# Kernel optimization log

Hardware: AMD Instinct MI355X
Metric: run time of the kernel (lower is better)

## Reference

```python
import jax, jax.numpy as jnp
import numpy as np

B, E, H, F, L, A = 256, 1024, 1024, 2048, 196, 512
C_RATIO, H_RATIO = 0.5, 0.5


def setup_inputs() -> dict:
    key = jax.random.key(0)
    ks = jax.random.split(key, 20)
    u = lambda k, shape: jax.random.uniform(k, shape, jnp.float32, -0.1, 0.1)
    return {
        "xt": jax.random.normal(ks[0], (B, E), jnp.float32),
        "att_seq": jax.random.normal(ks[1], (B, L, F), jnp.float32),
        "h": jax.random.normal(ks[2], (B, H), jnp.float32),
        "c": jax.random.normal(ks[3], (B, H), jnp.float32),
        "Wi": u(ks[4], (4 * H, E)), "bi": u(ks[5], (4 * H,)),
        "Wh": u(ks[6], (4 * H, H)), "bh": u(ks[7], (4 * H,)),
        "Wz": u(ks[8], (4 * H, F)), "bz": u(ks[9], (4 * H,)),
        "Wa": u(ks[10], (A, F)), "ba": u(ks[11], (A,)),
        "Wha": u(ks[12], (A, H)), "bha": u(ks[13], (A,)),
        "Wo": u(ks[14], (1, A)), "bo": u(ks[15], (1,)),
    }


def reference(xt, att_seq, h, c, Wi, bi, Wh, bh, Wz, bz, Wa, ba, Wha, bha, Wo, bo):
    # attention scoring: tanh(att_2_att_h(att) + h_2_att_h(h)) -> scalar per location
    att_linear = jnp.einsum("blf,af->bla", att_seq, Wa) + ba          # [B,L,A]
    h_linear = h @ Wha.T + bha                                        # [B,A]
    att_h = jnp.tanh(att_linear + h_linear[:, None, :])               # [B,L,A]
    scores = jnp.einsum("bla,a->bl", att_h, Wo[0]) + bo[0]            # [B,L]
    w = jax.nn.softmax(scores, axis=-1)                               # [B,L]
    z = jnp.einsum("bl,blf->bf", w, att_seq)                          # [B,F] context

    # fused LSTM gates
    sums = (xt @ Wi.T + bi) + (h @ Wh.T + bh) + (z @ Wz.T + bz)       # [B,4H]
    i_g = jax.nn.sigmoid(sums[:, 0 * H:1 * H])
    f_g = jax.nn.sigmoid(sums[:, 1 * H:2 * H])
    o_g = jax.nn.sigmoid(sums[:, 2 * H:3 * H])
    g = jnp.tanh(sums[:, 3 * H:4 * H])

    # zoneout blending (training mode; dropout prob is 0 -> identity)
    next_c = c * C_RATIO + (1.0 - C_RATIO) * (f_g * c + i_g * g)
    next_h = h * H_RATIO + (1.0 - H_RATIO) * (o_g * jnp.tanh(next_c))
    return next_h, next_h, next_c  # (output, state_h, state_c)
```

## Files before the change

### kernel.cpp

```cpp
#include <hip/hip_runtime.h>

#define B_ 256
#define E_ 1024
#define H_ 1024
#define F_ 2048
#define L_ 196
#define A_ 512
#define ML (B_ * L_)

typedef __attribute__((ext_vector_type(8))) short short8;
typedef __attribute__((ext_vector_type(4))) float f32x4;

__device__ __forceinline__ unsigned short f2bf(float x) {
  unsigned u = __float_as_uint(x);
  unsigned r = (u + 0x7FFFu + ((u >> 16) & 1u)) >> 16;
  return (unsigned short)r;
}
__device__ __forceinline__ float fast_tanh(float x) {
  x = fminf(fmaxf(x, -15.f), 15.f);
  float e = __expf(2.f * x);
  return (e - 1.f) / (e + 1.f);
}
__device__ __forceinline__ float sigmoidf_(float x) {
  return 1.f / (1.f + __expf(-x));
}

#define GLOAD_LDS(gptr, lptr) \
  __builtin_amdgcn_global_load_lds( \
      (const __attribute__((address_space(1))) void*)(gptr), \
      (__attribute__((address_space(3))) void*)(lptr), 16, 0, 0)

#define SBAR() asm volatile("s_barrier" ::: "memory")

__global__ void cast_wx_k(const float* __restrict__ Wa, const float* __restrict__ Wha,
                          const float* __restrict__ Wi, const float* __restrict__ Wh,
                          const float* __restrict__ Wz, const float* __restrict__ xt,
                          const float* __restrict__ h,
                          unsigned short* __restrict__ WaB, unsigned short* __restrict__ WhaB,
                          unsigned short* __restrict__ WgB, unsigned short* __restrict__ AgB) {
  size_t i = ((size_t)blockIdx.x * 256 + threadIdx.x) * 8;
  const float* src;
  unsigned short* dst;
  if (i < 1048576) { src = Wa + i; dst = WaB + i; }
  else if (i < 1572864) { src = Wha + (i - 1048576); dst = WhaB + (i - 1048576); }
  else if (i < 18350080) {
    size_t off = i - 1572864;
    int row = (int)(off >> 12), col = (int)(off & 4095);
    if (col < 1024)       src = Wi + (size_t)row * 1024 + col;
    else if (col < 2048)  src = Wh + (size_t)row * 1024 + (col - 1024);
    else                  src = Wz + (size_t)row * 2048 + (col - 2048);
    dst = WgB + off;
  } else {
    size_t off = i - 18350080;
    int row = (int)(off >> 11), col = (int)(off & 2047);
    src = (col < 1024) ? (xt + (size_t)row * 1024 + col) : (h + (size_t)row * 1024 + (col - 1024));
    dst = AgB + (size_t)row * 4096 + col;
  }
  float4 a = *reinterpret_cast<const float4*>(src);
  float4 b = *reinterpret_cast<const float4*>(src + 4);
  short8 o;
  o[0] = (short)f2bf(a.x); o[1] = (short)f2bf(a.y); o[2] = (short)f2bf(a.z); o[3] = (short)f2bf(a.w);
  o[4] = (short)f2bf(b.x); o[5] = (short)f2bf(b.y); o[6] = (short)f2bf(b.z); o[7] = (short)f2bf(b.w);
  *reinterpret_cast<short8*>(dst) = o;
}

__global__ __launch_bounds__(256, 2)
void hlin_gemm_k(const unsigned short* __restrict__ AgB, const unsigned short* __restrict__ WhaB,
                 const float* __restrict__ bha, float* __restrict__ hlin) {
  __shared__ unsigned short As[2][64 * 64];
  __shared__ unsigned short Bs[2][128 * 64];
  const int tid = threadIdx.x;
  const int lane = tid & 63, wid = tid >> 6;
  const int wm = wid >> 1, wn = wid & 1;
  const int m0 = blockIdx.y * 64;
  const int n0 = blockIdx.x * 128;
  const int g16 = lane >> 4, l16 = lane & 15;
  const int l7 = l16 & 7;
  f32x4 acc[2][4] = {};

#define STAGE_HL(BUF, KK)                                                                      \
  {                                                                                            \
    _Pragma("unroll")                                                                          \
    for (int it = 0; it < 2; ++it) {                                                           \
      int idx = it * 256 + tid;                                                                \
      int row = idx >> 3;                                                                      \
      int kc = (idx & 7) ^ (row & 7);                                                          \
      GLOAD_LDS(AgB + (size_t)(m0 + row) * 4096 + 1024 + (KK) + kc * 8, &As[BUF][idx * 8]);    \
    }                                                                                          \
    _Pragma("unroll")                                                                          \
    for (int it = 0; it < 4; ++it) {                                                           \
      int idx = it * 256 + tid;                                                                \
      int row = idx >> 3;                                                                      \
      int kc = (idx & 7) ^ (row & 7);                                                          \
      GLOAD_LDS(WhaB + (size_t)(n0 + row) * 1024 + (KK) + kc * 8, &Bs[BUF][idx * 8]);          \
    }                                                                                          \
  }

  STAGE_HL(0, 0);
  STAGE_HL(1, 64);
  asm volatile("s_waitcnt vmcnt(6)" ::: "memory");
  SBAR();
  int cur = 0;
  for (int k0 = 0; k0 < 1024; k0 += 64) {
    #pragma unroll
    for (int ks = 0; ks < 2; ++ks) {
      const int ko = ((ks * 4 + g16) ^ l7) << 3;
      short8 af[2], bfr[4];
      #pragma unroll
      for (int mi = 0; mi < 2; ++mi)
        af[mi] = *reinterpret_cast<const short8*>(&As[cur][(wm * 32 + mi * 16 + l16) * 64 + ko]);
      #pragma unroll
      for (int ni = 0; ni < 4; ++ni)
        bfr[ni] = *reinterpret_cast<const short8*>(&Bs[cur][(wn * 64 + ni * 16 + l16) * 64 + ko]);
      #pragma unroll
      for (int mi = 0; mi < 2; ++mi)
        #pragma unroll
        for (int ni = 0; ni < 4; ++ni)
          acc[mi][ni] = __builtin_amdgcn_mfma_f32_16x16x32_bf16(af[mi], bfr[ni], acc[mi][ni], 0, 0, 0);
    }
    SBAR();
    if (k0 + 128 < 1024) {
      STAGE_HL(cur, k0 + 128);
      asm volatile("s_waitcnt vmcnt(6)" ::: "memory");
    } else {
      asm volatile("s_waitcnt vmcnt(0)" ::: "memory");
    }
    SBAR();
    cur ^= 1;
  }
#undef STAGE_HL

  #pragma unroll
  for (int ni = 0; ni < 4; ++ni) {
    int col = n0 + wn * 64 + ni * 16 + l16;
    float bv = bha[col];
    #pragma unroll
    for (int mi = 0; mi < 2; ++mi)
      #pragma unroll
      for (int j = 0; j < 4; ++j) {
        int m = m0 + wm * 32 + mi * 16 + g16 * 4 + j;
        hlin[(size_t)m * A_ + col] = acc[mi][ni][j] + bv;
      }
  }
}

__global__ __launch_bounds__(512, 1)
void score_fuse_k(const float* __restrict__ att, const unsigned short* __restrict__ WaB,
                  const float* __restrict__ hlin, const float* __restrict__ ba,
                  const float* __restrict__ Wo, float* __restrict__ scores) {
  __shared__ unsigned short As[2][64 * 64];
  __shared__ unsigned short Bs[2][512 * 64];
  __shared__ float red[8][64];
  const int tid = threadIdx.x;
  const int lane = tid & 63, wn = tid >> 6;
  const int m0 = blockIdx.x * 64;
  const int g16 = lane >> 4, l16 = lane & 15;
  const int l7 = l16 & 7;
  f32x4 acc[4][4] = {};
  float4 R[2];

#define LOADA(KK)                                                                        \
  {                                                                                      \
    _Pragma("unroll")                                                                    \
    for (int it = 0; it < 2; ++it) {                                                     \
      int idx = it * 512 + tid;                                                          \
      int row = idx >> 4, kf = idx & 15;                                                 \
      R[it] = *reinterpret_cast<const float4*>(att + (size_t)(m0 + row) * F_ + (KK) + kf * 4); \
    }                                                                                    \
  }
#define GLDB(BUF, KK)                                                                    \
  {                                                                                      \
    _Pragma("unroll")                                                                    \
    for (int it = 0; it < 8; ++it) {                                                     \
      int idx = it * 512 + tid;                                                          \
      int row = idx >> 3;                                                                \
      int kc = (idx & 7) ^ (row & 7);                                                    \
      GLOAD_LDS(WaB + (size_t)row * F_ + (KK) + kc * 8, &Bs[BUF][idx * 8]);              \
    }                                                                                    \
  }
#define WRITEA(BUF)                                                                      \
  {                                                                                      \
    _Pragma("unroll")                                                                    \
    for (int it = 0; it < 2; ++it) {                                                     \
      int idx = it * 512 + tid;                                                          \
      int row = idx >> 4, kf = idx & 15;                                                 \
      float4 v = R[it];                                                                  \
      unsigned lo, hi;                                                                   \
      asm("v_cvt_pk_bf16_f32 %0, %1, %2" : "=v"(lo) : "v"(v.x), "v"(v.y));               \
      asm("v_cvt_pk_bf16_f32 %0, %1, %2" : "=v"(hi) : "v"(v.z), "v"(v.w));               \
      uint2 q; q.x = lo; q.y = hi;                                                       \
      int el = row * 64 + (((kf >> 1) ^ (row & 7)) << 3) + ((kf & 1) << 2);              \
      *reinterpret_cast<uint2*>(&As[BUF][el]) = q;                                       \
    }                                                                                    \
  }
#define COMPUTE(BUF)                                                                     \
  {                                                                                      \
    _Pragma("unroll")                                                                    \
    for (int ks = 0; ks < 2; ++ks) {                                                     \
      const int ko = ((ks * 4 + g16) ^ l7) << 3;                                         \
      short8 af[4], bfr[4];                                                              \
      _Pragma("unroll")                                                                  \
      for (int mi = 0; mi < 4; ++mi)                                                     \
        af[mi] = *reinterpret_cast<const short8*>(&As[BUF][(mi * 16 + l16) * 64 + ko]);  \
      _Pragma("unroll")                                                                  \
      for (int ni = 0; ni < 4; ++ni)                                                     \
        bfr[ni] = *reinterpret_cast<const short8*>(&Bs[BUF][(wn * 64 + ni * 16 + l16) * 64 + ko]); \
      _Pragma("unroll")                                                                  \
      for (int mi = 0; mi < 4; ++mi)                                                     \
        _Pragma("unroll")                                                                \
        for (int ni = 0; ni < 4; ++ni)                                                   \
          acc[mi][ni] = __builtin_amdgcn_mfma_f32_16x16x32_bf16(af[mi], bfr[ni], acc[mi][ni], 0, 0, 0); \
    }                                                                                    \
  }

  GLDB(0, 0);
  LOADA(0);
  asm volatile("s_waitcnt vmcnt(0)" ::: "memory");
  WRITEA(0);
  LOADA(64);
  GLDB(1, 64);
  asm volatile("s_waitcnt lgkmcnt(0)" ::: "memory");
  SBAR();

  int cur = 0;
  for (int t = 0; t < 32; ++t) {
    COMPUTE(cur);
    if (t + 1 < 32) WRITEA(cur ^ 1);
    SBAR();
    if (t + 2 < 32) {
      LOADA((t + 2) * 64);
      GLDB(cur, (t + 2) * 64);
      asm volatile("s_waitcnt vmcnt(10)" ::: "memory");
    } else {
      asm volatile("s_waitcnt vmcnt(0)" ::: "memory");
    }
    asm volatile("s_waitcnt lgkmcnt(0)" ::: "memory");
    SBAR();
    cur ^= 1;
  }
#undef LOADA
#undef GLDB
#undef WRITEA
#undef COMPUTE

  float wo_v[4], ba_v[4];
  int a_v[4];
  #pragma unroll
  for (int ni = 0; ni < 4; ++ni) {
    int a = wn * 64 + ni * 16 + l16;
    a_v[ni] = a; wo_v[ni] = Wo[a]; ba_v[ni] = ba[a];
  }
  #pragma unroll
  for (int mi = 0; mi < 4; ++mi) {
    float rs[4];
    #pragma unroll
    for (int j = 0; j < 4; ++j) {
      int m = m0 + mi * 16 + g16 * 4 + j;
      int b = m / L_;
      const float* hb = hlin + (size_t)b * A_;
      float s = 0.f;
      #pragma unroll
      for (int ni = 0; ni < 4; ++ni) {
        float v = acc[mi][ni][j] + ba_v[ni] + hb[a_v[ni]];
        s += fast_tanh(v) * wo_v[ni];
      }
      rs[j] = s;
    }
    #pragma unroll
    for (int off = 1; off < 16; off <<= 1) {
      #pragma unroll
      for (int j = 0; j < 4; ++j) rs[j] += __shfl_xor(rs[j], off);
    }
    if (l16 == 0) {
      #pragma unroll
      for (int j = 0; j < 4; ++j)
        red[wn][mi * 16 + g16 * 4 + j] = rs[j];
    }
  }
  __syncthreads();
  if (tid < 64) {
    float s = red[0][tid] + red[1][tid] + red[2][tid] + red[3][tid]
            + red[4][tid] + red[5][tid] + red[6][tid] + red[7][tid];
    scores[m0 + tid] = s;
  }
}

__global__ __launch_bounds__(256)
void z_sm_f32_k(const float* __restrict__ att, const float* __restrict__ scores,
                unsigned short* __restrict__ AgB) {
  __shared__ float sm[L_];
  const int b = blockIdx.y;
  const int tid = threadIdx.x;
  if (tid < L_) sm[tid] = scores[b * L_ + tid];
  __syncthreads();
  float mx = -1e30f;
  for (int l = 0; l < L_; ++l) mx = fmaxf(mx, sm[l]);
  float s = 0.f;
  for (int l = 0; l < L_; ++l) s += __expf(sm[l] - mx);
  const float inv = 1.f / s;
  __syncthreads();
  if (tid < L_) sm[tid] = __expf(sm[tid] - mx) * inv;
  __syncthreads();
  const int f0 = blockIdx.x * 1024 + tid * 4;
  const float* base = att + (size_t)b * L_ * F_ + f0;
  float a0 = 0.f, a1 = 0.f, a2 = 0.f, a3 = 0.f;
  #pragma unroll 4
  for (int l = 0; l < L_; ++l) {
    float wl = sm[l];
    float4 a = *reinterpret_cast<const float4*>(base + (size_t)l * F_);
    a0 += wl * a.x; a1 += wl * a.y; a2 += wl * a.z; a3 += wl * a.w;
  }
  ushort4 o;
  o.x = f2bf(a0); o.y = f2bf(a1); o.z = f2bf(a2); o.w = f2bf(a3);
  *reinterpret_cast<ushort4*>(AgB + (size_t)b * 4096 + 2048 + f0) = o;
}

__global__ __launch_bounds__(256, 4)
void gates_gemm_k(const unsigned short* __restrict__ AgB, const unsigned short* __restrict__ WgB,
                  const float* __restrict__ bi, const float* __restrict__ bh,
                  const float* __restrict__ bz, float* __restrict__ sums) {
  __shared__ unsigned short As[2][64 * 64];
  __shared__ unsigned short Bs[2][64 * 64];
  const int tid = threadIdx.x;
  const int lane = tid & 63, wid = tid >> 6;
  const int wm = wid >> 1, wn = wid & 1;
  const int m0 = blockIdx.y * 64;
  const int n0 = blockIdx.x * 64;
  const int g16 = lane >> 4, l16 = lane & 15;
  const int l7 = l16 & 7;
  f32x4 acc[2][2] = {};

#define STAGE_GG(BUF, KK)                                                               \
  {                                                                                     \
    _Pragma("unroll")                                                                   \
    for (int it = 0; it < 2; ++it) {                                                    \
      int idx = it * 256 + tid;                                                         \
      int row = idx >> 3;                                                               \
      int kc = (idx & 7) ^ (row & 7);                                                   \
      GLOAD_LDS(AgB + (size_t)(m0 + row) * 4096 + (KK) + kc * 8, &As[BUF][idx * 8]);    \
      GLOAD_LDS(WgB + (size_t)(n0 + row) * 4096 + (KK) + kc * 8, &Bs[BUF][idx * 8]);    \
    }                                                                                   \
  }

  STAGE_GG(0, 0);
  STAGE_GG(1, 64);
  asm volatile("s_waitcnt vmcnt(4)" ::: "memory");
  SBAR();
  int cur = 0;
  for (int k0 = 0; k0 < 4096; k0 += 64) {
    #pragma unroll
    for (int ks = 0; ks < 2; ++ks) {
      const int ko = ((ks * 4 + g16) ^ l7) << 3;
      short8 af[2], bfr[2];
      #pragma unroll
      for (int mi = 0; mi < 2; ++mi)
        af[mi] = *reinterpret_cast<const short8*>(&As[cur][(wm * 32 + mi * 16 + l16) * 64 + ko]);
      #pragma unroll
      for (int ni = 0; ni < 2; ++ni)
        bfr[ni] = *reinterpret_cast<const short8*>(&Bs[cur][(wn * 32 + ni * 16 + l16) * 64 + ko]);
      #pragma unroll
      for (int mi = 0; mi < 2; ++mi)
        #pragma unroll
        for (int ni = 0; ni < 2; ++ni)
          acc[mi][ni] = __builtin_amdgcn_mfma_f32_16x16x32_bf16(af[mi], bfr[ni], acc[mi][ni], 0, 0, 0);
    }
    SBAR();
    if (k0 + 128 < 4096) {
      STAGE_GG(cur, k0 + 128);
      asm volatile("s_waitcnt vmcnt(4)" ::: "memory");
    } else {
      asm volatile("s_waitcnt vmcnt(0)" ::: "memory");
    }
    SBAR();
    cur ^= 1;
  }
#undef STAGE_GG

  #pragma unroll
  for (int ni = 0; ni < 2; ++ni) {
    int col = n0 + wn * 32 + ni * 16 + l16;
    float bsum = bi[col] + bh[col] + bz[col];
    #pragma unroll
    for (int mi = 0; mi < 2; ++mi)
      #pragma unroll
      for (int j = 0; j < 4; ++j) {
        int m = m0 + wm * 32 + mi * 16 + g16 * 4 + j;
        sums[(size_t)m * 4096 + col] = acc[mi][ni][j] + bsum;
      }
  }
}

__global__ void final_k(const float* __restrict__ sums, const float* __restrict__ h,
                        const float* __restrict__ c, float* __restrict__ out) {
  int i = blockIdx.x * 256 + threadIdx.x;
  int b = i >> 10, hh = i & 1023;
  const float* srow = sums + (size_t)b * 4096;
  float ig = sigmoidf_(srow[hh]);
  float fg = sigmoidf_(srow[1024 + hh]);
  float og = sigmoidf_(srow[2048 + hh]);
  float g  = fast_tanh(srow[3072 + hh]);
  float cv = c[i], hv = h[i];
  float nc = 0.5f * cv + 0.5f * (fg * cv + ig * g);
  float nh = 0.5f * hv + 0.5f * (og * fast_tanh(nc));
  out[i] = nh;
  out[B_ * H_ + i] = nh;
  out[2 * B_ * H_ + i] = nc;
}

extern "C" void kernel_launch(void* const* d_in, const int* in_sizes, int n_in,
                              void* d_out, int out_size, void* d_ws, size_t ws_size,
                              hipStream_t stream) {
  const float* xt  = (const float*)d_in[0];
  const float* att = (const float*)d_in[1];
  const float* h   = (const float*)d_in[2];
  const float* c   = (const float*)d_in[3];
  const float* Wi  = (const float*)d_in[4];
  const float* bi  = (const float*)d_in[5];
  const float* Wh  = (const float*)d_in[6];
  const float* bh  = (const float*)d_in[7];
  const float* Wz  = (const float*)d_in[8];
  const float* bz  = (const float*)d_in[9];
  const float* Wa  = (const float*)d_in[10];
  const float* ba  = (const float*)d_in[11];
  const float* Wha = (const float*)d_in[12];
  const float* bha = (const float*)d_in[13];
  const float* Wo  = (const float*)d_in[14];

  char* ws = (char*)d_ws;
  const size_t MB = (size_t)1 << 20;
  unsigned short* WaB  = (unsigned short*)(ws);
  unsigned short* WhaB = (unsigned short*)(ws + 2 * MB);
  unsigned short* WgB  = (unsigned short*)(ws + 3 * MB);
  unsigned short* AgB  = (unsigned short*)(ws + 35 * MB);
  float* hlin    = (float*)(ws + 37 * MB);
  float* scores  = (float*)(ws + 38 * MB);
  float* sums    = (float*)(ws + 40 * MB);
  float* out = (float*)d_out;

  cast_wx_k<<<9216, 256, 0, stream>>>(Wa, Wha, Wi, Wh, Wz, xt, h, WaB, WhaB, WgB, AgB);
  hlin_gemm_k<<<dim3(4, 4), 256, 0, stream>>>(AgB, WhaB, bha, hlin);
  score_fuse_k<<<ML / 64, 512, 0, stream>>>(att, WaB, hlin, ba, Wo, scores);
  z_sm_f32_k<<<dim3(2, B_), 256, 0, stream>>>(att, scores, AgB);
  gates_gemm_k<<<dim3(64, 4), 256, 0, stream>>>(AgB, WgB, bi, bh, bz, sums);
  final_k<<<B_ * H_ / 256, 256, 0, stream>>>(sums, h, c, out);
}
```

Before: 414.2 us.

## Single-buffer Wa tile in score kernel to fit two blocks per CU

The B (Wa) shared-memory tile in the attention score GEMM kernel drops from double to single buffering, and the reduction scratch is aliased onto the A buffer. Together these cut shared memory enough that launch bounds can ask for two 512-thread blocks per CU. The load schedule is reordered so the B tile for the next step is fetched after the compute barrier, with A still prefetched two steps ahead. The intent is to hide latency with a second resident block instead of intra-block double buffering. The cost is that each block now stalls on the B fetch between steps, and the tighter register budget could cause spills.

```diff
diff --git a/kernel.cpp b/kernel.cpp
--- a/kernel.cpp
+++ b/kernel.cpp
@@ -144,13 +144,12 @@
   }
 }
 
-__global__ __launch_bounds__(512, 1)
+__global__ __launch_bounds__(512, 2)
 void score_fuse_k(const float* __restrict__ att, const unsigned short* __restrict__ WaB,
                   const float* __restrict__ hlin, const float* __restrict__ ba,
                   const float* __restrict__ Wo, float* __restrict__ scores) {
   __shared__ unsigned short As[2][64 * 64];
-  __shared__ unsigned short Bs[2][512 * 64];
-  __shared__ float red[8][64];
+  __shared__ unsigned short Bs[512 * 64];
   const int tid = threadIdx.x;
   const int lane = tid & 63, wn = tid >> 6;
   const int m0 = blockIdx.x * 64;
@@ -168,14 +167,14 @@
       R[it] = *reinterpret_cast<const float4*>(att + (size_t)(m0 + row) * F_ + (KK) + kf * 4); \
     }                                                                                    \
   }
-#define GLDB(BUF, KK)                                                                    \
+#define GLDB(KK)                                                                         \
   {                                                                                      \
     _Pragma("unroll")                                                                    \
     for (int it = 0; it < 8; ++it) {                                                     \
       int idx = it * 512 + tid;                                                          \
       int row = idx >> 3;                                                                \
       int kc = (idx & 7) ^ (row & 7);                                                    \
-      GLOAD_LDS(WaB + (size_t)row * F_ + (KK) + kc * 8, &Bs[BUF][idx * 8]);              \
+      GLOAD_LDS(WaB + (size_t)row * F_ + (KK) + kc * 8, &Bs[idx * 8]);                   \
     }                                                                                    \
   }
 #define WRITEA(BUF)                                                                      \
@@ -204,7 +203,7 @@
         af[mi] = *reinterpret_cast<const short8*>(&As[BUF][(mi * 16 + l16) * 64 + ko]);  \
       _Pragma("unroll")                                                                  \
       for (int ni = 0; ni < 4; ++ni)                                                     \
-        bfr[ni] = *reinterpret_cast<const short8*>(&Bs[BUF][(wn * 64 + ni * 16 + l16) * 64 + ko]); \
+        bfr[ni] = *reinterpret_cast<const short8*>(&Bs[(wn * 64 + ni * 16 + l16) * 64 + ko]); \
       _Pragma("unroll")                                                                  \
       for (int mi = 0; mi < 4; ++mi)                                                     \
         _Pragma("unroll")                                                                \
@@ -213,36 +212,38 @@
     }                                                                                    \
   }
 
-  GLDB(0, 0);
   LOADA(0);
-  asm volatile("s_waitcnt vmcnt(0)" ::: "memory");
+  GLDB(0);
+  asm volatile("s_waitcnt vmcnt(8)" ::: "memory");
   WRITEA(0);
   LOADA(64);
-  GLDB(1, 64);
+  asm volatile("s_waitcnt vmcnt(2)" ::: "memory");
   asm volatile("s_waitcnt lgkmcnt(0)" ::: "memory");
   SBAR();
 
-  int cur = 0;
   for (int t = 0; t < 32; ++t) {
-    COMPUTE(cur);
-    if (t + 1 < 32) WRITEA(cur ^ 1);
+    COMPUTE(t & 1);
     SBAR();
-    if (t + 2 < 32) {
-      LOADA((t + 2) * 64);
-      GLDB(cur, (t + 2) * 64);
-      asm volatile("s_waitcnt vmcnt(10)" ::: "memory");
-    } else {
-      asm volatile("s_waitcnt vmcnt(0)" ::: "memory");
-    }
-    asm volatile("s_waitcnt lgkmcnt(0)" ::: "memory");
-    SBAR();
-    cur ^= 1;
+    if (t + 1 < 32) {
+      GLDB((t + 1) * 64);
+      asm volatile("s_waitcnt vmcnt(8)" ::: "memory");
+      WRITEA((t + 1) & 1);
+      if (t + 2 < 32) {
+        LOADA((t + 2) * 64);
+        asm volatile("s_waitcnt vmcnt(2)" ::: "memory");
+      } else {
+        asm volatile("s_waitcnt vmcnt(0)" ::: "memory");
+      }
+      asm volatile("s_waitcnt lgkmcnt(0)" ::: "memory");
+      SBAR();
+    }
   }
 #undef LOADA
 #undef GLDB
 #undef WRITEA
 #undef COMPUTE
 
+  float* red = (float*)&As[0][0];
   float wo_v[4], ba_v[4];
   int a_v[4];
   #pragma unroll
@@ -274,13 +275,14 @@
     if (l16 == 0) {
       #pragma unroll
       for (int j = 0; j < 4; ++j)
-        red[wn][mi * 16 + g16 * 4 + j] = rs[j];
+        red[wn * 64 + mi * 16 + g16 * 4 + j] = rs[j];
     }
   }
   __syncthreads();
   if (tid < 64) {
-    float s = red[0][tid] + red[1][tid] + red[2][tid] + red[3][tid]
-            + red[4][tid] + red[5][tid] + red[6][tid] + red[7][tid];
+    float s = 0.f;
+    #pragma unroll
+    for (int w = 0; w < 8; ++w) s += red[w * 64 + tid];
     scores[m0 + tid] = s;
   }
 }
```

Measured after the change: 421.9 us. About the same (+1.9%).
